# Optimization experiments

Measured on AMD Instinct MI355X. Metric: run time of the kernel, lower is better.

Reference implementation:

```python
import jax, jax.numpy as jnp
import numpy as np

N_HEAD = 12

def setup_inputs() -> dict:
    key = jax.random.key(0)
    ks = jax.random.split(key, 3)
    B, T, D = 4, 2048, 768
    x = jax.random.normal(ks[0], (B, T, D), dtype=jnp.float32)
    W_qkv = jax.random.normal(ks[1], (D, 3 * D), dtype=jnp.float32) * (1.0 / np.sqrt(D))
    b_qkv = jnp.zeros((3 * D,), dtype=jnp.float32)
    W_o = jax.random.normal(ks[2], (D, D), dtype=jnp.float32) * (1.0 / np.sqrt(D))
    b_o = jnp.zeros((D,), dtype=jnp.float32)
    return {"x": x, "W_qkv": W_qkv, "b_qkv": b_qkv, "W_o": W_o, "b_o": b_o}


def reference(x, W_qkv, b_qkv, W_o, b_o):
    B, T, D = x.shape
    H = N_HEAD
    hd = D // H
    qkv = x @ W_qkv + b_qkv                      # [B,T,3D]
    q, k, v = jnp.split(qkv, 3, axis=-1)
    # [B,T,D] -> [B,H,T,hd]
    q = q.reshape(B, T, H, hd).transpose(0, 2, 1, 3)
    k = k.reshape(B, T, H, hd).transpose(0, 2, 1, 3)
    v = v.reshape(B, T, H, hd).transpose(0, 2, 1, 3)
    scale = 1.0 / np.sqrt(hd).astype(np.float32)
    scores = jnp.einsum('bhqd,bhkd->bhqk', q, k) * scale   # [B,H,T,T]
    causal = jnp.tril(jnp.ones((T, T), dtype=bool))
    scores = jnp.where(causal[None, None, :, :], scores, -jnp.inf)
    attn = jax.nn.softmax(scores, axis=-1)
    out = jnp.einsum('bhqk,bhkd->bhqd', attn, v)            # [B,H,T,hd]
    out = out.transpose(0, 2, 1, 3).reshape(B, T, D)
    return out @ W_o + b_o
```

## Files before the change

### kernel.cpp

```cpp
#include <hip/hip_runtime.h>
#include <hip/hip_bf16.h>

typedef __bf16 bf16_t;
typedef float f32x4 __attribute__((ext_vector_type(4)));
typedef bf16_t bf16x8 __attribute__((ext_vector_type(8)));
typedef bf16_t bf16x4 __attribute__((ext_vector_type(4)));

#define MFMA16(a, b, c) __builtin_amdgcn_mfma_f32_16x16x32_bf16(a, b, c, 0, 0, 0)

#define QSCALE 0.18033688011112042f

__device__ __forceinline__ void gl_lds16(const bf16_t* g, bf16_t* l) {
    __builtin_amdgcn_global_load_lds(
        (const __attribute__((address_space(1))) unsigned int*)g,
        (__attribute__((address_space(3))) unsigned int*)l, 16, 0, 0);
}

__device__ __forceinline__ float fexp2(float x) {
    float y;
    asm("v_exp_f32 %0, %1" : "=v"(y) : "v"(x));
    return y;
}

__device__ __forceinline__ void conv_t_body(const float* __restrict__ in,
                                            bf16_t* __restrict__ out,
                                            int R, int C, int bx, int by,
                                            float (*t)[33]) {
    const int tx = threadIdx.x & 31;
    const int ty = threadIdx.x >> 5;
#pragma unroll
    for (int i = 0; i < 4; i++)
        t[ty + i * 8][tx] = in[(size_t)(by + ty + i * 8) * C + bx + tx];
    __syncthreads();
#pragma unroll
    for (int i = 0; i < 4; i++)
        out[(size_t)(bx + ty + i * 8) * R + by + tx] = (bf16_t)t[tx][ty + i * 8];
}

__global__ __launch_bounds__(256) void prep_k(
    const float* __restrict__ x,    bf16_t* __restrict__ xb,
    const float* __restrict__ Wqkv, bf16_t* __restrict__ Wt,
    const float* __restrict__ Wo,   bf16_t* __restrict__ Wot)
{
    __shared__ float t[32][33];
    const int blk = blockIdx.x;
    if (blk < 6144) {
        const int i = (blk * 256 + threadIdx.x) * 4;
        float4 v = *(const float4*)(x + i);
        bf16x4 o = { (bf16_t)v.x, (bf16_t)v.y, (bf16_t)v.z, (bf16_t)v.w };
        *(bf16x4*)(xb + i) = o;
    } else if (blk < 7872) {
        const int idx = blk - 6144;
        conv_t_body(Wqkv, Wt, 768, 2304, (idx % 72) * 32, (idx / 72) * 32, t);
    } else {
        const int idx = blk - 7872;
        conv_t_body(Wo, Wot, 768, 768, (idx % 24) * 32, (idx / 24) * 32, t);
    }
}

__global__ __launch_bounds__(256) void vtrans(const bf16_t* __restrict__ Vp,
                                              bf16_t* __restrict__ Vt) {
    __shared__ __align__(16) bf16_t Ts[64 * 72];
    const int t0 = blockIdx.x * 64;
    const int bh = blockIdx.y;
    const int r  = threadIdx.x >> 2;
    const int cb = (threadIdx.x & 3) * 16;
    const bf16_t* src = Vp + (((size_t)bh * 2048 + t0 + r) << 6) + cb;
    *(bf16x8*)(Ts + r * 72 + cb)     = *(const bf16x8*)(src);
    *(bf16x8*)(Ts + r * 72 + cb + 8) = *(const bf16x8*)(src + 8);
    __syncthreads();
    const int f  = threadIdx.x >> 2;
    const int tb = (threadIdx.x & 3) * 16;
    bf16_t* dst = Vt + (((size_t)bh * 64 + f) << 11) + t0 + tb;
    bf16x8 a, b;
#pragma unroll
    for (int i = 0; i < 8; i++) a[i] = Ts[(tb + i) * 72 + f];
#pragma unroll
    for (int i = 0; i < 8; i++) b[i] = Ts[(tb + 8 + i) * 72 + f];
    *(bf16x8*)(dst)     = a;
    *(bf16x8*)(dst + 8) = b;
}

template <int EPI>
__global__ __launch_bounds__(256) void gemm_bt(
    const bf16_t* __restrict__ A, const bf16_t* __restrict__ Bt,
    const float* __restrict__ bias,
    void* __restrict__ O0v, bf16_t* __restrict__ O1, bf16_t* __restrict__ O2,
    int M, int N, int K)
{
    __shared__ __align__(16) bf16_t As[2][128 * 32];
    __shared__ __align__(16) bf16_t Bs[2][128 * 32];

    const int tid  = threadIdx.x;
    const int wid  = tid >> 6;
    const int lane = tid & 63;
    const int quad = lane >> 4;
    const int l15  = lane & 15;
    const int wm   = (wid >> 1) * 64;
    const int wn   = (wid & 1) * 64;
    const int qs8  = (quad ^ ((l15 >> 1) & 3)) * 8;

    const int mtiles = M >> 7;
    const int mtpx   = mtiles >> 3;
    const int bid    = blockIdx.x;
    const int xcd    = bid & 7;
    const int slot   = bid >> 3;
    const int m0     = (xcd * mtpx + (slot % mtpx)) << 7;
    const int n0     = (slot / mtpx) << 7;

    f32x4 acc[4][4];
#pragma unroll
    for (int i = 0; i < 4; i++)
#pragma unroll
        for (int j = 0; j < 4; j++) acc[i][j] = (f32x4){0.f, 0.f, 0.f, 0.f};

    const int srow = tid >> 2;
    const int scol = (((tid & 3) ^ ((srow >> 1) & 3)) ) * 8;
    const bf16_t* ag0 = A  + (size_t)(m0 + srow) * K + scol;
    const bf16_t* ag1 = A  + (size_t)(m0 + 64 + srow) * K + scol;
    const bf16_t* bg0 = Bt + (size_t)(n0 + srow) * K + scol;
    const bf16_t* bg1 = Bt + (size_t)(n0 + 64 + srow) * K + scol;

    auto prefetch = [&](int k0, int buf) {
        gl_lds16(ag0 + k0, As[buf] + tid * 8);
        gl_lds16(ag1 + k0, As[buf] + 2048 + tid * 8);
        gl_lds16(bg0 + k0, Bs[buf] + tid * 8);
        gl_lds16(bg1 + k0, Bs[buf] + 2048 + tid * 8);
    };

    const int niter = K >> 5;
    prefetch(0, 0);
    for (int i = 0; i < niter; i++) {
        __syncthreads();
        if (i + 1 < niter) prefetch((i + 1) << 5, (i + 1) & 1);
        const bf16_t* Ap = As[i & 1];
        const bf16_t* Bp = Bs[i & 1];

        bf16x8 af[4], bfr[4];
#pragma unroll
        for (int ii = 0; ii < 4; ii++)
            af[ii] = *(const bf16x8*)(Ap + (wm + ii * 16 + l15) * 32 + qs8);
#pragma unroll
        for (int j = 0; j < 4; j++)
            bfr[j] = *(const bf16x8*)(Bp + (wn + j * 16 + l15) * 32 + qs8);
#pragma unroll
        for (int ii = 0; ii < 4; ii++)
#pragma unroll
            for (int j = 0; j < 4; j++)
                acc[ii][j] = MFMA16(af[ii], bfr[j], acc[ii][j]);
    }

    if (EPI == 0) {
        const int sec = n0 / 768;
        const float scale = (sec == 0) ? QSCALE : 1.f;
        bf16_t* dst = (sec == 0) ? (bf16_t*)O0v : (sec == 1 ? O1 : O2);
#pragma unroll
        for (int i = 0; i < 4; i++) {
            const int mbase = m0 + wm + i * 16 + quad * 4;
#pragma unroll
            for (int j = 0; j < 4; j++) {
                const int n  = n0 + wn + j * 16 + l15;
                const float bv = bias[n];
                const int d    = n - sec * 768;
                const int h    = d >> 6;
                const int feat = d & 63;
#pragma unroll
                for (int r = 0; r < 4; r++) {
                    const int mm = mbase + r;
                    const int b  = mm >> 11;
                    const int tt = mm & 2047;
                    const int bh = b * 12 + h;
                    dst[(((size_t)bh * 2048 + tt) << 6) + feat] =
                        (bf16_t)((acc[i][j][r] + bv) * scale);
                }
            }
        }
    } else {
#pragma unroll
        for (int i = 0; i < 4; i++) {
            const int mbase = m0 + wm + i * 16 + quad * 4;
#pragma unroll
            for (int j = 0; j < 4; j++) {
                const int n  = n0 + wn + j * 16 + l15;
                const float bv = bias[n];
#pragma unroll
                for (int r = 0; r < 4; r++)
                    ((float*)O0v)[(size_t)(mbase + r) * N + n] = acc[i][j][r] + bv;
            }
        }
    }
}

__global__ __launch_bounds__(256, 3) void attn_k(
    const bf16_t* __restrict__ Q, const bf16_t* __restrict__ Kb,
    const bf16_t* __restrict__ Vt, bf16_t* __restrict__ AO)
{
    __shared__ __align__(16) bf16_t Ks[2 * 4096];
    __shared__ __align__(16) bf16_t Vs[2 * 4096];
    __shared__ __align__(16) bf16_t Ps[4 * 2048];

    const int tid  = threadIdx.x;
    const int wid  = tid >> 6;
    const int lane = tid & 63;
    const int quad = lane >> 4;
    const int l15  = lane & 15;
    const int qs8  = (quad ^ ((l15 >> 1) & 3)) * 8;

    const int bid  = blockIdx.x;
    const int xcd  = bid & 7;
    const int slot = bid >> 3;
    const int bh   = xcd * 6 + (slot % 6);
    const int qt2  = 15 - (slot / 6);
    const int q0   = qt2 << 7;

    const bf16_t* Qb  = Q  + ((size_t)bh << 17);
    const bf16_t* Kbh = Kb + ((size_t)bh << 17);
    const bf16_t* Vbh = Vt + ((size_t)bh << 17);

    bf16_t* Pw = Ps + wid * 2048;
    const int swl = l15 & 7;
    bf16_t* pwr[2][4];
    const bf16_t* prd[2][2];
#pragma unroll
    for (int g = 0; g < 2; g++) {
#pragma unroll
        for (int c = 0; c < 4; c++)
            pwr[g][c] = Pw + g * 1024 + l15 * 64 +
                        (((((c << 1) | (quad >> 1))) ^ swl) << 3) + ((quad & 1) << 2);
#pragma unroll
        for (int kk = 0; kk < 2; kk++)
            prd[g][kk] = Pw + g * 1024 + l15 * 64 + ((((kk << 2) | quad) ^ swl) << 3);
    }

    const bf16x8 ones = { (bf16_t)1.f, (bf16_t)1.f, (bf16_t)1.f, (bf16_t)1.f,
                          (bf16_t)1.f, (bf16_t)1.f, (bf16_t)1.f, (bf16_t)1.f };

    const int srow = tid >> 2;
    const int scol = (((tid & 3) ^ ((srow >> 1) & 3))) * 8;

    auto prefetch = [&](int j, int buf) {
        const int kv0 = j * 64;
        bf16_t* kd = Ks + buf * 4096 + tid * 8;
        bf16_t* vd = Vs + buf * 4096 + tid * 8;
#pragma unroll
        for (int c = 0; c < 2; c++) {
            gl_lds16(Kbh + (size_t)(kv0 + srow) * 64 + c * 32 + scol, kd + c * 2048);
            gl_lds16(Vbh + (size_t)srow * 2048 + kv0 + c * 32 + scol, vd + c * 2048);
        }
    };

    const int b = bh / 12;
    const int h = bh - b * 12;

    const int qg0 = q0 + wid * 16 + l15;
    const int qg1 = qg0 + 64;

    bf16x8 qf[2][2];
#pragma unroll
    for (int g = 0; g < 2; g++) {
        const bf16_t* qp = Qb + ((size_t)(g ? qg1 : qg0) << 6) + quad * 8;
        qf[g][0] = *(const bf16x8*)(qp);
        qf[g][1] = *(const bf16x8*)(qp + 32);
    }

    f32x4 lacc[2];
    f32x4 oacc[2][4];
#pragma unroll
    for (int g = 0; g < 2; g++) {
        lacc[g] = (f32x4){0.f, 0.f, 0.f, 0.f};
#pragma unroll
        for (int f = 0; f < 4; f++) oacc[g][f] = (f32x4){0.f, 0.f, 0.f, 0.f};
    }

    const int cnt = 2 * qt2 + 2;
    prefetch(0, 0);

    for (int i = 0; i < cnt; i++) {
        __syncthreads();
        if (i + 1 < cnt) prefetch(i + 1, (i + 1) & 1);
        const bf16_t* Kp = Ks + (i & 1) * 4096;
        const bf16_t* Vp = Vs + (i & 1) * 4096;

        f32x4 st[2][4];
        __builtin_amdgcn_s_setprio(1);
#pragma unroll
        for (int c = 0; c < 4; c++) {
            st[0][c] = (f32x4){0.f, 0.f, 0.f, 0.f};
            st[1][c] = (f32x4){0.f, 0.f, 0.f, 0.f};
#pragma unroll
            for (int kk = 0; kk < 2; kk++) {
                bf16x8 kf = *(const bf16x8*)(Kp + kk * 2048 + (c * 16 + l15) * 32 + qs8);
                st[0][c] = MFMA16(kf, qf[0][kk], st[0][c]);
                st[1][c] = MFMA16(kf, qf[1][kk], st[1][c]);
            }
        }
        __builtin_amdgcn_s_setprio(0);

        const int kvb = i * 64 + quad * 4;
        if (i >= 2 * qt2) {
#pragma unroll
            for (int c = 0; c < 4; c++)
#pragma unroll
                for (int r = 0; r < 4; r++)
                    if (kvb + c * 16 + r > qg0) st[0][c][r] = -3e38f;
            if (i == 2 * qt2 + 1) {
#pragma unroll
                for (int c = 0; c < 4; c++)
#pragma unroll
                    for (int r = 0; r < 4; r++)
                        if (kvb + c * 16 + r > qg1) st[1][c][r] = -3e38f;
            }
        }

#pragma unroll
        for (int g = 0; g < 2; g++)
#pragma unroll
            for (int c = 0; c < 4; c++) {
                bf16x4 pk = { (bf16_t)fexp2(st[g][c][0]), (bf16_t)fexp2(st[g][c][1]),
                              (bf16_t)fexp2(st[g][c][2]), (bf16_t)fexp2(st[g][c][3]) };
                *(bf16x4*)pwr[g][c] = pk;
            }

        bf16x8 pb[2][2];
#pragma unroll
        for (int g = 0; g < 2; g++)
#pragma unroll
            for (int kk = 0; kk < 2; kk++)
                pb[g][kk] = *(const bf16x8*)prd[g][kk];

        __builtin_amdgcn_s_setprio(1);
        lacc[0] = MFMA16(ones, pb[0][0], lacc[0]);
        lacc[0] = MFMA16(ones, pb[0][1], lacc[0]);
        lacc[1] = MFMA16(ones, pb[1][0], lacc[1]);
        lacc[1] = MFMA16(ones, pb[1][1], lacc[1]);

#pragma unroll
        for (int f = 0; f < 4; f++)
#pragma unroll
            for (int kk = 0; kk < 2; kk++) {
                bf16x8 vf = *(const bf16x8*)(Vp + kk * 2048 + (f * 16 + l15) * 32 + qs8);
                oacc[0][f] = MFMA16(vf, pb[0][kk], oacc[0][f]);
                oacc[1][f] = MFMA16(vf, pb[1][kk], oacc[1][f]);
            }
        __builtin_amdgcn_s_setprio(0);
    }

#pragma unroll
    for (int g = 0; g < 2; g++) {
        const float inv = 1.0f / lacc[g][0];
        const int qg = g ? qg1 : qg0;
        bf16_t* dst = AO + ((size_t)(b * 2048 + qg)) * 768 + h * 64 + quad * 4;
#pragma unroll
        for (int f = 0; f < 4; f++) {
            bf16x4 o = { (bf16_t)(oacc[g][f][0] * inv), (bf16_t)(oacc[g][f][1] * inv),
                         (bf16_t)(oacc[g][f][2] * inv), (bf16_t)(oacc[g][f][3] * inv) };
            *(bf16x4*)(dst + f * 16) = o;
        }
    }
}

extern "C" void kernel_launch(void* const* d_in, const int* in_sizes, int n_in,
                              void* d_out, int out_size, void* d_ws, size_t ws_size,
                              hipStream_t stream)
{
    const float* x    = (const float*)d_in[0];
    const float* Wqkv = (const float*)d_in[1];
    const float* bqkv = (const float*)d_in[2];
    const float* Wo   = (const float*)d_in[3];
    const float* bo   = (const float*)d_in[4];
    float* out = (float*)d_out;

    const size_t per = (size_t)48 * 2048 * 64;
    bf16_t* Qs  = (bf16_t*)d_ws;
    bf16_t* Kk  = Qs + per;
    bf16_t* Vt  = Kk + per;
    bf16_t* AO  = Vt + per;
    bf16_t* xb  = AO + per;
    bf16_t* Wt  = xb + per;
    bf16_t* Wot = Wt + (size_t)2304 * 768;
    bf16_t* Vpl = (bf16_t*)d_out;

    prep_k<<<8448, 256, 0, stream>>>(x, xb, Wqkv, Wt, Wo, Wot);

    gemm_bt<0><<<18 * 64, 256, 0, stream>>>(
        xb, Wt, bqkv, (void*)Qs, Kk, Vpl, 8192, 2304, 768);
    vtrans<<<dim3(32, 48), 256, 0, stream>>>(Vpl, Vt);
    attn_k<<<768, 256, 0, stream>>>(Qs, Kk, Vt, AO);
    gemm_bt<1><<<6 * 64, 256, 0, stream>>>(
        AO, Wot, bo, (void*)out, nullptr, nullptr, 8192, 768, 768);
}
```

Baseline: 196.5 us.

## Fuse V transpose into QKV GEMM epilogue and rebalance attention block schedule

The QKV GEMM epilogue now writes the V section straight into the feature-major transposed layout, packing four consecutive tokens per bf16x4 store. This removes the separate vtrans kernel launch and its round trip through the scratch buffer. The attention kernel's block-to-(head, query-tile) mapping is replaced by hardcoded nibble tables that aim to balance causal work across rounds of blocks. In exchange, the V stores become strided across rows and the schedule depends on the fixed 768-block grid shape.

```diff
diff --git a/kernel.cpp b/kernel.cpp
--- a/kernel.cpp
+++ b/kernel.cpp
@@ -58,29 +58,6 @@
     }
 }
 
-__global__ __launch_bounds__(256) void vtrans(const bf16_t* __restrict__ Vp,
-                                              bf16_t* __restrict__ Vt) {
-    __shared__ __align__(16) bf16_t Ts[64 * 72];
-    const int t0 = blockIdx.x * 64;
-    const int bh = blockIdx.y;
-    const int r  = threadIdx.x >> 2;
-    const int cb = (threadIdx.x & 3) * 16;
-    const bf16_t* src = Vp + (((size_t)bh * 2048 + t0 + r) << 6) + cb;
-    *(bf16x8*)(Ts + r * 72 + cb)     = *(const bf16x8*)(src);
-    *(bf16x8*)(Ts + r * 72 + cb + 8) = *(const bf16x8*)(src + 8);
-    __syncthreads();
-    const int f  = threadIdx.x >> 2;
-    const int tb = (threadIdx.x & 3) * 16;
-    bf16_t* dst = Vt + (((size_t)bh * 64 + f) << 11) + t0 + tb;
-    bf16x8 a, b;
-#pragma unroll
-    for (int i = 0; i < 8; i++) a[i] = Ts[(tb + i) * 72 + f];
-#pragma unroll
-    for (int i = 0; i < 8; i++) b[i] = Ts[(tb + 8 + i) * 72 + f];
-    *(bf16x8*)(dst)     = a;
-    *(bf16x8*)(dst + 8) = b;
-}
-
 template <int EPI>
 __global__ __launch_bounds__(256) void gemm_bt(
     const bf16_t* __restrict__ A, const bf16_t* __restrict__ Bt,
@@ -152,26 +129,47 @@
 
     if (EPI == 0) {
         const int sec = n0 / 768;
-        const float scale = (sec == 0) ? QSCALE : 1.f;
-        bf16_t* dst = (sec == 0) ? (bf16_t*)O0v : (sec == 1 ? O1 : O2);
-#pragma unroll
-        for (int i = 0; i < 4; i++) {
-            const int mbase = m0 + wm + i * 16 + quad * 4;
-#pragma unroll
-            for (int j = 0; j < 4; j++) {
-                const int n  = n0 + wn + j * 16 + l15;
-                const float bv = bias[n];
-                const int d    = n - sec * 768;
-                const int h    = d >> 6;
-                const int feat = d & 63;
-#pragma unroll
-                for (int r = 0; r < 4; r++) {
-                    const int mm = mbase + r;
-                    const int b  = mm >> 11;
-                    const int tt = mm & 2047;
-                    const int bh = b * 12 + h;
-                    dst[(((size_t)bh * 2048 + tt) << 6) + feat] =
-                        (bf16_t)((acc[i][j][r] + bv) * scale);
+        if (sec < 2) {
+            const float scale = (sec == 0) ? QSCALE : 1.f;
+            bf16_t* dst = (sec == 0) ? (bf16_t*)O0v : O1;
+#pragma unroll
+            for (int i = 0; i < 4; i++) {
+                const int mbase = m0 + wm + i * 16 + quad * 4;
+#pragma unroll
+                for (int j = 0; j < 4; j++) {
+                    const int n  = n0 + wn + j * 16 + l15;
+                    const float bv = bias[n];
+                    const int d    = n - sec * 768;
+                    const int h    = d >> 6;
+                    const int feat = d & 63;
+#pragma unroll
+                    for (int r = 0; r < 4; r++) {
+                        const int mm = mbase + r;
+                        const int b  = mm >> 11;
+                        const int tt = mm & 2047;
+                        const int bh = b * 12 + h;
+                        dst[(((size_t)bh * 2048 + tt) << 6) + feat] =
+                            (bf16_t)((acc[i][j][r] + bv) * scale);
+                    }
+                }
+            }
+        } else {
+#pragma unroll
+            for (int i = 0; i < 4; i++) {
+                const int mbase = m0 + wm + i * 16 + quad * 4;
+                const int bb = mbase >> 11;
+                const int tt = mbase & 2047;
+#pragma unroll
+                for (int j = 0; j < 4; j++) {
+                    const int n  = n0 + wn + j * 16 + l15;
+                    const float bv = bias[n];
+                    const int d    = n - 1536;
+                    const int h    = d >> 6;
+                    const int feat = d & 63;
+                    const int bh   = bb * 12 + h;
+                    bf16x4 o = { (bf16_t)(acc[i][j][0] + bv), (bf16_t)(acc[i][j][1] + bv),
+                                 (bf16_t)(acc[i][j][2] + bv), (bf16_t)(acc[i][j][3] + bv) };
+                    *(bf16x4*)(O2 + (((size_t)bh * 64 + feat) << 11) + tt) = o;
                 }
             }
         }
@@ -206,12 +204,22 @@
     const int l15  = lane & 15;
     const int qs8  = (quad ^ ((l15 >> 1) & 3)) * 8;
 
-    const int bid  = blockIdx.x;
-    const int xcd  = bid & 7;
-    const int slot = bid >> 3;
-    const int bh   = xcd * 6 + (slot % 6);
-    const int qt2  = 15 - (slot / 6);
-    const int q0   = qt2 << 7;
+    const int bid = blockIdx.x;
+    const int r3  = bid >> 8;
+    const int jj  = bid & 255;
+    const int m   = jj & 15;
+    const int u   = jj >> 4;
+    const unsigned long long ordT = (r3 == 0) ? 0xABBBCCCDDDEEEFFFULL
+                                  : (r3 == 1) ? 0x968A79A789568567ULL
+                                              : 0x3541421210430320ULL;
+    const unsigned long long occT = (r3 == 0) ? 0x2210210210210210ULL
+                                  : (r3 == 1) ? 0x2221210110110000ULL
+                                              : 0x2222121102011000ULL;
+    const int ord = (int)((ordT >> (4 * m)) & 15);
+    const int occ = (int)((occT >> (4 * m)) & 15);
+    const int bh  = u + (occ << 4);
+    const int qt2 = 15 - ord;
+    const int q0  = qt2 << 7;
 
     const bf16_t* Qb  = Q  + ((size_t)bh << 17);
     const bf16_t* Kbh = Kb + ((size_t)bh << 17);
@@ -378,13 +386,11 @@
     bf16_t* xb  = AO + per;
     bf16_t* Wt  = xb + per;
     bf16_t* Wot = Wt + (size_t)2304 * 768;
-    bf16_t* Vpl = (bf16_t*)d_out;
 
     prep_k<<<8448, 256, 0, stream>>>(x, xb, Wqkv, Wt, Wo, Wot);
 
     gemm_bt<0><<<18 * 64, 256, 0, stream>>>(
-        xb, Wt, bqkv, (void*)Qs, Kk, Vpl, 8192, 2304, 768);
-    vtrans<<<dim3(32, 48), 256, 0, stream>>>(Vpl, Vt);
+        xb, Wt, bqkv, (void*)Qs, Kk, Vt, 8192, 2304, 768);
     attn_k<<<768, 256, 0, stream>>>(Qs, Kk, Vt, AO);
     gemm_bt<1><<<6 * 64, 256, 0, stream>>>(
         AO, Wot, bo, (void*)out, nullptr, nullptr, 8192, 768, 768);
```

Measured after the change: 196.4 us. Within noise of the previous version (-0.0%).
